# Performance work log

Hardware: AMD Instinct MI355X
Metric: run time of the kernel (lower is better)

Reference implementation:

```python
import jax, jax.numpy as jnp
import numpy as np

B, D, P, V = 8192, 128, 64, 32000  # batch, penultimate_dim, n_patterns, vocab


def setup_inputs() -> dict:
    key = jax.random.key(0)
    ks = jax.random.split(key, 8)
    return {
        "x": jax.random.normal(ks[0], (B, D), dtype=jnp.float32),
        "pattern_dict": jax.random.normal(ks[1], (P, D), dtype=jnp.float32) / np.sqrt(D),
        "attn_w": jax.random.normal(ks[2], (D, P), dtype=jnp.float32) / np.sqrt(D),
        "attn_b": jnp.zeros((P,), dtype=jnp.float32),
        "self_w": jax.random.normal(ks[3], (D, D), dtype=jnp.float32) / np.sqrt(D),
        "self_b": jnp.zeros((D,), dtype=jnp.float32),
        "out_w": jax.random.normal(ks[4], (D, V), dtype=jnp.float32) / np.sqrt(D),
        "out_b": jnp.zeros((V,), dtype=jnp.float32),
    }


def reference(x, pattern_dict, attn_w, attn_b, self_w, self_b, out_w, out_b):
    # pattern attention over codebook: [B,D] @ [D,P] -> softmax over P
    pattern_weights = jax.nn.softmax(x @ attn_w + attn_b, axis=-1)  # [B,P]
    # reconstruction from codebook: [B,P] @ [P,D]
    rec = pattern_weights @ pattern_dict  # [B,D]
    # self-predictor paradox gate
    self_pred = rec @ self_w + self_b  # [B,D]
    paradox = self_pred - rec
    paradox_mag = jnp.linalg.norm(paradox, axis=-1, keepdims=True)  # [B,1]
    gated = rec * jax.nn.sigmoid(paradox_mag)  # [B,D]
    # output projection to vocab
    return gated @ out_w + out_b  # [B,V]
```

## Files before the change

### kernel.cpp

```cpp
#include <hip/hip_runtime.h>
#include <hip/hip_bf16.h>

#define BATCH 8192
#define DIM   128
#define NPAT  64
#define VOCAB 32000
#define CHUNKS (BATCH / 16)

#define NPANEL  125
#define NSPLITS 8
#define CPB     (CHUNKS / NSPLITS)

typedef __attribute__((ext_vector_type(8))) short short8;
typedef __attribute__((ext_vector_type(4))) float f32x4;

__global__ __launch_bounds__(256) void phaseA_kernel(
    const float* __restrict__ x,
    const float* __restrict__ attn_w,
    const float* __restrict__ attn_b,
    const float* __restrict__ pattern_dict,
    const float* __restrict__ self_w,
    const float* __restrict__ self_b,
    __hip_bfloat16* __restrict__ gated)
{
    __shared__ float xs[4][DIM];
    __shared__ float wls[4][NPAT];
    __shared__ float recs[4][DIM];

    const int lane = threadIdx.x & 63;
    const int wid  = threadIdx.x >> 6;
    const int row  = blockIdx.x * 4 + wid;

    xs[wid][lane]      = x[row * DIM + lane];
    xs[wid][lane + 64] = x[row * DIM + 64 + lane];
    __syncthreads();

    float acc = attn_b[lane];
#pragma unroll 8
    for (int d = 0; d < DIM; ++d)
        acc += xs[wid][d] * attn_w[d * NPAT + lane];

    float m = acc;
#pragma unroll
    for (int o = 32; o; o >>= 1) m = fmaxf(m, __shfl_xor(m, o));
    float e = expf(acc - m);
    float s = e;
#pragma unroll
    for (int o = 32; o; o >>= 1) s += __shfl_xor(s, o);
    float w = e / s;
    wls[wid][lane] = w;
    __syncthreads();

    float r0 = 0.f, r1 = 0.f;
#pragma unroll 8
    for (int p = 0; p < NPAT; ++p) {
        float wp = wls[wid][p];
        r0 += wp * pattern_dict[p * DIM + lane];
        r1 += wp * pattern_dict[p * DIM + 64 + lane];
    }
    recs[wid][lane]      = r0;
    recs[wid][lane + 64] = r1;
    __syncthreads();

    float s0 = self_b[lane], s1 = self_b[lane + 64];
#pragma unroll 8
    for (int k = 0; k < DIM; ++k) {
        float rk = recs[wid][k];
        s0 += rk * self_w[k * DIM + lane];
        s1 += rk * self_w[k * DIM + 64 + lane];
    }

    float p0 = s0 - r0, p1 = s1 - r1;
    float ss = p0 * p0 + p1 * p1;
#pragma unroll
    for (int o = 32; o; o >>= 1) ss += __shfl_xor(ss, o);
    float mag = sqrtf(ss);
    float g = 1.f / (1.f + expf(-mag));

    gated[row * DIM + lane]      = __float2bfloat16(r0 * g);
    gated[row * DIM + 64 + lane] = __float2bfloat16(r1 * g);
}

__global__ __launch_bounds__(256) void repack_a_kernel(
    const __hip_bfloat16* __restrict__ gated,
    __hip_bfloat16* __restrict__ Af)
{
    const int lane = threadIdx.x & 63;
    const int wv   = threadIdx.x >> 6;
    const int ch   = blockIdx.x * 4 + wv;
    const int r16  = lane & 15;
    const int kq   = lane >> 4;
#pragma unroll
    for (int ks = 0; ks < 4; ++ks) {
        short8 v = *reinterpret_cast<const short8*>(
            gated + (size_t)(ch * 16 + r16) * DIM + ks * 32 + kq * 8);
        *reinterpret_cast<short8*>(
            Af + ((size_t)(ch * 4 + ks) * 64 + lane) * 8) = v;
    }
}

__global__ __launch_bounds__(256) void repack_w_kernel(
    const float* __restrict__ out_w,
    __hip_bfloat16* __restrict__ Bf)
{
    __shared__ __hip_bfloat16 tile[64][136];

    const int t  = threadIdx.x;
    const int n0 = blockIdx.x * 64;
    const int c  = t & 63;
    const int k0 = t >> 6;

    for (int kk = 0; kk < DIM; kk += 4) {
        int k = kk + k0;
        tile[c][k] = __float2bfloat16(out_w[(size_t)k * VOCAB + n0 + c]);
    }
    __syncthreads();

    const int lane = t & 63;
    const int tl   = t >> 6;
    const int r16  = lane & 15;
    const int kq   = lane >> 4;
    const int gt   = (n0 >> 4) + tl;
#pragma unroll
    for (int ks = 0; ks < 4; ++ks) {
        uint4 v = *reinterpret_cast<const uint4*>(&tile[tl * 16 + r16][ks * 32 + kq * 8]);
        *reinterpret_cast<uint4*>(Bf + ((size_t)(gt * 4 + ks) * 64 + lane) * 8) = v;
    }
}

__global__ __launch_bounds__(128, 2) void gemm_kernel(
    const __hip_bfloat16* __restrict__ Af,
    const __hip_bfloat16* __restrict__ Bf,
    const float* __restrict__ bias,
    float* __restrict__ out)
{
    __shared__ char epi[2][8192];

    const int lane  = threadIdx.x & 63;
    const int w     = threadIdx.x >> 6;
    const int r16   = lane & 15;
    const int kq    = lane >> 4;
    const int rr    = lane >> 5;
    const int l31   = lane & 31;
    const int panel = blockIdx.x % NPANEL;
    const int split = blockIdx.x / NPANEL;
    const int col0  = panel * 256 + w * 128;
    const int t0    = panel * 16 + w * 8;
    const int ch0   = split * CPB;

    short8 b[8][4];
#pragma unroll
    for (int t = 0; t < 8; ++t)
#pragma unroll
        for (int ks = 0; ks < 4; ++ks)
            b[t][ks] = *reinterpret_cast<const short8*>(
                Bf + ((size_t)((t0 + t) * 4 + ks) * 64 + lane) * 8);

    const f32x4 bb = *reinterpret_cast<const f32x4*>(bias + col0 + l31 * 4);

    char* pad = &epi[w][0];

    auto aload = [&](int ch, short8* a) {
#pragma unroll
        for (int ks = 0; ks < 4; ++ks)
            a[ks] = *reinterpret_cast<const short8*>(
                Af + ((size_t)(ch * 4 + ks) * 64 + lane) * 8);
    };

    short8 a0[4], a1[4];
    aload(ch0, a0);

#pragma unroll 2
    for (int c = 0; c < CPB; ++c) {
        short8* acur = (c & 1) ? a1 : a0;
        short8* anxt = (c & 1) ? a0 : a1;
        const int ch = ch0 + c;

        if (c + 1 < CPB) aload(ch + 1, anxt);

        f32x4 acc[8];
#pragma unroll
        for (int t = 0; t < 8; ++t) {
            f32x4 z = {};
#pragma unroll
            for (int ks = 0; ks < 4; ++ks)
                z = __builtin_amdgcn_mfma_f32_16x16x32_bf16(
                    b[t][ks], acur[ks], z, 0, 0, 0);
            acc[t] = z;
        }

#pragma unroll
        for (int t = 0; t < 8; ++t) {
            const int pb = r16 * 512 + ((t * 64 + kq * 16) ^ ((r16 & 7) << 4));
            *reinterpret_cast<f32x4*>(pad + pb) = acc[t];
        }

        const size_t orow0 = (size_t)ch * 16 * VOCAB + col0;
#pragma unroll
        for (int s = 0; s < 8; ++s) {
            const int row = 2 * s + rr;
            const int pb  = row * 512 + ((l31 * 16) ^ ((row & 7) << 4));
            f32x4 v = *reinterpret_cast<const f32x4*>(pad + pb);
            v += bb;
            *reinterpret_cast<f32x4*>(out + orow0 + (size_t)row * VOCAB + l31 * 4) = v;
        }
    }
}

extern "C" void kernel_launch(void* const* d_in, const int* in_sizes, int n_in,
                              void* d_out, int out_size, void* d_ws, size_t ws_size,
                              hipStream_t stream) {
    const float* x            = (const float*)d_in[0];
    const float* pattern_dict = (const float*)d_in[1];
    const float* attn_w       = (const float*)d_in[2];
    const float* attn_b       = (const float*)d_in[3];
    const float* self_w       = (const float*)d_in[4];
    const float* self_b       = (const float*)d_in[5];
    const float* out_w        = (const float*)d_in[6];
    const float* out_b        = (const float*)d_in[7];
    float* out = (float*)d_out;

    __hip_bfloat16* gated = (__hip_bfloat16*)d_ws;
    __hip_bfloat16* Af    = (__hip_bfloat16*)((char*)d_ws + (size_t)BATCH * DIM * 2);
    __hip_bfloat16* Bf    = (__hip_bfloat16*)((char*)d_ws + (size_t)2 * BATCH * DIM * 2);

    phaseA_kernel<<<BATCH / 4, 256, 0, stream>>>(
        x, attn_w, attn_b, pattern_dict, self_w, self_b, gated);
    repack_a_kernel<<<CHUNKS / 4, 256, 0, stream>>>(gated, Af);
    repack_w_kernel<<<VOCAB / 64, 256, 0, stream>>>(out_w, Bf);
    gemm_kernel<<<NPANEL * NSPLITS, 128, 0, stream>>>(Af, Bf, out_b, out);
}
```

Before: 244.6 us.

## Fuse phase-A, A-repack and W-repack into one prep kernel

Merges the three preprocessing kernels into a single launch. Phase-A blocks now write the gated rows directly into the MFMA fragment layout through shared memory, so the intermediate gated buffer and its repack pass go away. The W-repack runs as extra blocks of the same grid, concurrently with phase-A. This cuts two kernel launches and one global round trip, at the cost of heavier shared-memory use per block and a single wave doing the tiny Af store.

Measured after the change: 240.6 us. About the same (-1.6%).

```diff
diff --git a/kernel.cpp b/kernel.cpp
--- a/kernel.cpp
+++ b/kernel.cpp
@@ -11,120 +11,118 @@
 #define NSPLITS 8
 #define CPB     (CHUNKS / NSPLITS)
 
+#define PA_BLOCKS 2048
+#define RW_BLOCKS (VOCAB / 64)
+
 typedef __attribute__((ext_vector_type(8))) short short8;
 typedef __attribute__((ext_vector_type(4))) float f32x4;
 
-__global__ __launch_bounds__(256) void phaseA_kernel(
+__global__ __launch_bounds__(256) void prep_kernel(
     const float* __restrict__ x,
     const float* __restrict__ attn_w,
     const float* __restrict__ attn_b,
     const float* __restrict__ pattern_dict,
     const float* __restrict__ self_w,
     const float* __restrict__ self_b,
-    __hip_bfloat16* __restrict__ gated)
-{
-    __shared__ float xs[4][DIM];
-    __shared__ float wls[4][NPAT];
-    __shared__ float recs[4][DIM];
-
-    const int lane = threadIdx.x & 63;
-    const int wid  = threadIdx.x >> 6;
-    const int row  = blockIdx.x * 4 + wid;
-
-    xs[wid][lane]      = x[row * DIM + lane];
-    xs[wid][lane + 64] = x[row * DIM + 64 + lane];
-    __syncthreads();
-
-    float acc = attn_b[lane];
-#pragma unroll 8
-    for (int d = 0; d < DIM; ++d)
-        acc += xs[wid][d] * attn_w[d * NPAT + lane];
-
-    float m = acc;
-#pragma unroll
-    for (int o = 32; o; o >>= 1) m = fmaxf(m, __shfl_xor(m, o));
-    float e = expf(acc - m);
-    float s = e;
-#pragma unroll
-    for (int o = 32; o; o >>= 1) s += __shfl_xor(s, o);
-    float w = e / s;
-    wls[wid][lane] = w;
-    __syncthreads();
-
-    float r0 = 0.f, r1 = 0.f;
-#pragma unroll 8
-    for (int p = 0; p < NPAT; ++p) {
-        float wp = wls[wid][p];
-        r0 += wp * pattern_dict[p * DIM + lane];
-        r1 += wp * pattern_dict[p * DIM + 64 + lane];
-    }
-    recs[wid][lane]      = r0;
-    recs[wid][lane + 64] = r1;
-    __syncthreads();
-
-    float s0 = self_b[lane], s1 = self_b[lane + 64];
-#pragma unroll 8
-    for (int k = 0; k < DIM; ++k) {
-        float rk = recs[wid][k];
-        s0 += rk * self_w[k * DIM + lane];
-        s1 += rk * self_w[k * DIM + 64 + lane];
-    }
-
-    float p0 = s0 - r0, p1 = s1 - r1;
-    float ss = p0 * p0 + p1 * p1;
-#pragma unroll
-    for (int o = 32; o; o >>= 1) ss += __shfl_xor(ss, o);
-    float mag = sqrtf(ss);
-    float g = 1.f / (1.f + expf(-mag));
-
-    gated[row * DIM + lane]      = __float2bfloat16(r0 * g);
-    gated[row * DIM + 64 + lane] = __float2bfloat16(r1 * g);
-}
-
-__global__ __launch_bounds__(256) void repack_a_kernel(
-    const __hip_bfloat16* __restrict__ gated,
-    __hip_bfloat16* __restrict__ Af)
-{
-    const int lane = threadIdx.x & 63;
-    const int wv   = threadIdx.x >> 6;
-    const int ch   = blockIdx.x * 4 + wv;
-    const int r16  = lane & 15;
-    const int kq   = lane >> 4;
-#pragma unroll
-    for (int ks = 0; ks < 4; ++ks) {
-        short8 v = *reinterpret_cast<const short8*>(
-            gated + (size_t)(ch * 16 + r16) * DIM + ks * 32 + kq * 8);
-        *reinterpret_cast<short8*>(
-            Af + ((size_t)(ch * 4 + ks) * 64 + lane) * 8) = v;
-    }
-}
-
-__global__ __launch_bounds__(256) void repack_w_kernel(
     const float* __restrict__ out_w,
+    __hip_bfloat16* __restrict__ Af,
     __hip_bfloat16* __restrict__ Bf)
 {
-    __shared__ __hip_bfloat16 tile[64][136];
-
-    const int t  = threadIdx.x;
-    const int n0 = blockIdx.x * 64;
-    const int c  = t & 63;
-    const int k0 = t >> 6;
-
-    for (int kk = 0; kk < DIM; kk += 4) {
-        int k = kk + k0;
-        tile[c][k] = __float2bfloat16(out_w[(size_t)k * VOCAB + n0 + c]);
-    }
-    __syncthreads();
-
-    const int lane = t & 63;
-    const int tl   = t >> 6;
-    const int r16  = lane & 15;
-    const int kq   = lane >> 4;
-    const int gt   = (n0 >> 4) + tl;
-#pragma unroll
-    for (int ks = 0; ks < 4; ++ks) {
-        uint4 v = *reinterpret_cast<const uint4*>(&tile[tl * 16 + r16][ks * 32 + kq * 8]);
-        *reinterpret_cast<uint4*>(Bf + ((size_t)(gt * 4 + ks) * 64 + lane) * 8) = v;
+    if (blockIdx.x < PA_BLOCKS) {
+        __shared__ float xs[4][DIM];
+        __shared__ float wls[4][NPAT];
+        __shared__ float recs[4][DIM];
+        __shared__ __hip_bfloat16 gs[4][136];
+
+        const int lane = threadIdx.x & 63;
+        const int wid  = threadIdx.x >> 6;
+        const int bidx = blockIdx.x;
+        const int row  = bidx * 4 + wid;
+
+        xs[wid][lane]      = x[row * DIM + lane];
+        xs[wid][lane + 64] = x[row * DIM + 64 + lane];
+        __syncthreads();
+
+        float acc = attn_b[lane];
+#pragma unroll 8
+        for (int d = 0; d < DIM; ++d)
+            acc += xs[wid][d] * attn_w[d * NPAT + lane];
+
+        float m = acc;
+#pragma unroll
+        for (int o = 32; o; o >>= 1) m = fmaxf(m, __shfl_xor(m, o));
+        float e = expf(acc - m);
+        float s = e;
+#pragma unroll
+        for (int o = 32; o; o >>= 1) s += __shfl_xor(s, o);
+        float w = e / s;
+        wls[wid][lane] = w;
+        __syncthreads();
+
+        float r0 = 0.f, r1 = 0.f;
+#pragma unroll 8
+        for (int p = 0; p < NPAT; ++p) {
+            float wp = wls[wid][p];
+            r0 += wp * pattern_dict[p * DIM + lane];
+            r1 += wp * pattern_dict[p * DIM + 64 + lane];
+        }
+        recs[wid][lane]      = r0;
+        recs[wid][lane + 64] = r1;
+        __syncthreads();
+
+        float s0 = self_b[lane], s1 = self_b[lane + 64];
+#pragma unroll 8
+        for (int k = 0; k < DIM; ++k) {
+            float rk = recs[wid][k];
+            s0 += rk * self_w[k * DIM + lane];
+            s1 += rk * self_w[k * DIM + 64 + lane];
+        }
+
+        float p0 = s0 - r0, p1 = s1 - r1;
+        float ss = p0 * p0 + p1 * p1;
+#pragma unroll
+        for (int o = 32; o; o >>= 1) ss += __shfl_xor(ss, o);
+        float mag = sqrtf(ss);
+        float g = 1.f / (1.f + expf(-mag));
+
+        gs[wid][lane]      = __float2bfloat16(r0 * g);
+        gs[wid][lane + 64] = __float2bfloat16(r1 * g);
+        __syncthreads();
+
+        if (wid == 0) {
+            const int ch      = bidx >> 2;
+            const int r16base = (bidx & 3) * 4;
+            const int ks    = lane >> 4;
+            const int kq    = (lane >> 2) & 3;
+            const int wid_r = lane & 3;
+            uint4 v = *reinterpret_cast<const uint4*>(&gs[wid_r][ks * 32 + kq * 8]);
+            *reinterpret_cast<uint4*>(
+                Af + ((size_t)((ch * 4 + ks) * 64 + kq * 16 + r16base + wid_r)) * 8) = v;
+        }
+    } else {
+        __shared__ __hip_bfloat16 tile[64][136];
+
+        const int t  = threadIdx.x;
+        const int n0 = (blockIdx.x - PA_BLOCKS) * 64;
+        const int c  = t & 63;
+        const int k0 = t >> 6;
+
+        for (int kk = 0; kk < DIM; kk += 4) {
+            int k = kk + k0;
+            tile[c][k] = __float2bfloat16(out_w[(size_t)k * VOCAB + n0 + c]);
+        }
+        __syncthreads();
+
+        const int lane = t & 63;
+        const int tl   = t >> 6;
+        const int r16  = lane & 15;
+        const int kq   = lane >> 4;
+        const int gt   = (n0 >> 4) + tl;
+#pragma unroll
+        for (int ks = 0; ks < 4; ++ks) {
+            uint4 v = *reinterpret_cast<const uint4*>(&tile[tl * 16 + r16][ks * 32 + kq * 8]);
+            *reinterpret_cast<uint4*>(Bf + ((size_t)(gt * 4 + ks) * 64 + lane) * 8) = v;
+        }
     }
 }
 
@@ -220,13 +218,10 @@
     const float* out_b        = (const float*)d_in[7];
     float* out = (float*)d_out;
 
-    __hip_bfloat16* gated = (__hip_bfloat16*)d_ws;
-    __hip_bfloat16* Af    = (__hip_bfloat16*)((char*)d_ws + (size_t)BATCH * DIM * 2);
-    __hip_bfloat16* Bf    = (__hip_bfloat16*)((char*)d_ws + (size_t)2 * BATCH * DIM * 2);
-
-    phaseA_kernel<<<BATCH / 4, 256, 0, stream>>>(
-        x, attn_w, attn_b, pattern_dict, self_w, self_b, gated);
-    repack_a_kernel<<<CHUNKS / 4, 256, 0, stream>>>(gated, Af);
-    repack_w_kernel<<<VOCAB / 64, 256, 0, stream>>>(out_w, Bf);
+    __hip_bfloat16* Af = (__hip_bfloat16*)d_ws;
+    __hip_bfloat16* Bf = (__hip_bfloat16*)((char*)d_ws + (size_t)BATCH * DIM * 2);
+
+    prep_kernel<<<PA_BLOCKS + RW_BLOCKS, 256, 0, stream>>>(
+        x, attn_w, attn_b, pattern_dict, self_w, self_b, out_w, Af, Bf);
     gemm_kernel<<<NPANEL * NSPLITS, 128, 0, stream>>>(Af, Bf, out_b, out);
 }
```
